# Optimization experiments

Measured on AMD Instinct MI355X. Metric: run time of the kernel, lower is better.

## Reference

```python
import jax, jax.numpy as jnp
import numpy as np

N_NODES = 40000
FEAT = 128
HID = 128
EMB = 64
N_EDGES = 640000


def setup_inputs() -> dict:
    key = jax.random.key(0)
    ks = jax.random.split(key, 8)
    x = jax.random.normal(ks[0], (N_NODES, FEAT), dtype=jnp.float32)
    edge_index = jax.random.randint(ks[1], (2, N_EDGES), 0, N_NODES, dtype=jnp.int64)
    s1 = 1.0 / np.sqrt(FEAT)
    s2 = 1.0 / np.sqrt(HID)
    W1_l = jax.random.uniform(ks[2], (HID, FEAT), jnp.float32, -s1, s1)
    b1 = jax.random.uniform(ks[3], (HID,), jnp.float32, -s1, s1)
    W1_r = jax.random.uniform(ks[4], (HID, FEAT), jnp.float32, -s1, s1)
    W2_l = jax.random.uniform(ks[5], (EMB, HID), jnp.float32, -s2, s2)
    b2 = jax.random.uniform(ks[6], (EMB,), jnp.float32, -s2, s2)
    W2_r = jax.random.uniform(ks[7], (EMB, HID), jnp.float32, -s2, s2)
    return {"x": x, "edge_index": edge_index, "W1_l": W1_l, "b1": b1,
            "W1_r": W1_r, "W2_l": W2_l, "b2": b2, "W2_r": W2_r}


def _sage_conv(x, src, dst, W_l, b_l, W_r, n_nodes):
    # mean aggregation of source-node features onto destination nodes
    msg = x[src]                                           # [E, d]
    agg = jax.ops.segment_sum(msg, dst, num_segments=n_nodes)   # [N, d]
    cnt = jax.ops.segment_sum(jnp.ones((src.shape[0],), x.dtype), dst,
                              num_segments=n_nodes)        # [N]
    agg = agg / jnp.maximum(cnt, 1.0)[:, None]
    # out = lin_l(mean_j x_j) + lin_r(x_i); bias lives in lin_l
    return agg @ W_l.T + b_l + x @ W_r.T


def reference(x, edge_index, W1_l, b1, W1_r, W2_l, b2, W2_r):
    src, dst = edge_index[0], edge_index[1]
    n = x.shape[0]
    h = _sage_conv(x, src, dst, W1_l, b1, W1_r, n)
    h = jax.nn.elu(h)
    # dropout p=0.2 is identity in eval mode
    h = _sage_conv(h, src, dst, W2_l, b2, W2_r, n)
    return jax.nn.log_softmax(h, axis=1)
```

## Files before the change

kernel.cpp:

```cpp
#include <hip/hip_runtime.h>
#include <hip/hip_fp16.h>
#include <math.h>

#define N_NODES 40000
#define FEATD 128
#define EMB 64
#define N_EDGES 640000
#define CAP 64
#define NB 79
#define BINCAP 10240

typedef unsigned short u16;
typedef unsigned char u8;
typedef unsigned int u32;
typedef __attribute__((ext_vector_type(8))) unsigned short u16x8;
typedef __attribute__((ext_vector_type(8))) _Float16 f16x8;
typedef __attribute__((ext_vector_type(4))) float f32x4;
typedef __attribute__((ext_vector_type(2))) float f32x2;
typedef __attribute__((ext_vector_type(2))) unsigned int u32x2;

__device__ __forceinline__ float h2f(u16 h) {
  __half hh;
  *(u16*)&hh = h;
  return __half2float(hh);
}
__device__ __forceinline__ u16 f2h(float f) {
  __half hh = __float2half(f);
  return *(u16*)&hh;
}

__global__ __launch_bounds__(256) void prep_fill_kernel(
    const float* __restrict__ x, const float* __restrict__ W1l,
    const float* __restrict__ W1r, const float* __restrict__ W2l,
    const float* __restrict__ W2r, const int* __restrict__ src,
    const int* __restrict__ dst, u16* __restrict__ xh, u8* __restrict__ xq,
    u16* __restrict__ wp, u32* __restrict__ binstore, int* __restrict__ binCnt) {
  __shared__ int hist[NB], starts[NB + 1], cnt2[NB], gbase[NB];
  __shared__ u32 staging[1024];
  int bid = blockIdx.x;
  int tid = threadIdx.x;
  if (bid < 625) {
    if (tid < NB) { hist[tid] = 0; cnt2[tid] = 0; }
    __syncthreads();
    int t = bid * 256 + tid;
    int4 s4 = *(const int4*)(&src[t * 4]);
    int4 d4 = *(const int4*)(&dst[t * 4]);
    int b0 = d4.x >> 9, b1 = d4.y >> 9, b2 = d4.z >> 9, b3 = d4.w >> 9;
    atomicAdd(&hist[b0], 1); atomicAdd(&hist[b1], 1);
    atomicAdd(&hist[b2], 1); atomicAdd(&hist[b3], 1);
    __syncthreads();
    if (tid == 0) {
      int run = 0;
      for (int i = 0; i < NB; i++) { starts[i] = run; run += hist[i]; }
      starts[NB] = run;
    }
    __syncthreads();
    u32 e0 = ((u32)d4.x << 16) | (u32)s4.x;
    u32 e1 = ((u32)d4.y << 16) | (u32)s4.y;
    u32 e2 = ((u32)d4.z << 16) | (u32)s4.z;
    u32 e3 = ((u32)d4.w << 16) | (u32)s4.w;
    int p0 = starts[b0] + atomicAdd(&cnt2[b0], 1); staging[p0] = e0;
    int p1 = starts[b1] + atomicAdd(&cnt2[b1], 1); staging[p1] = e1;
    int p2 = starts[b2] + atomicAdd(&cnt2[b2], 1); staging[p2] = e2;
    int p3 = starts[b3] + atomicAdd(&cnt2[b3], 1); staging[p3] = e3;
    __syncthreads();
    if (tid < NB) gbase[tid] = atomicAdd(&binCnt[tid * 16], hist[tid]);
    __syncthreads();
#pragma unroll
    for (int it = 0; it < 4; it++) {
      int i = tid + 256 * it;
      u32 e = staging[i];
      int b = (int)(e >> 25);
      int g = gbase[b] + (i - starts[b]);
      if (g < BINCAP) binstore[(size_t)b * BINCAP + g] = e;
    }
  } else if (bid < 3125) {
    int i = (bid - 625) * 256 + tid;
    float4 v0 = *(const float4*)(&x[i * 8]);
    float4 v1 = *(const float4*)(&x[i * 8 + 4]);
    u16x8 o;
    o[0] = f2h(v0.x); o[1] = f2h(v0.y); o[2] = f2h(v0.z); o[3] = f2h(v0.w);
    o[4] = f2h(v1.x); o[5] = f2h(v1.y); o[6] = f2h(v1.z); o[7] = f2h(v1.w);
    *(u16x8*)(&xh[i * 8]) = o;
    u32 w0 = __builtin_amdgcn_cvt_pk_fp8_f32(v0.x, v0.y, 0u, false);
    w0 = __builtin_amdgcn_cvt_pk_fp8_f32(v0.z, v0.w, w0, true);
    u32 w1 = __builtin_amdgcn_cvt_pk_fp8_f32(v1.x, v1.y, 0u, false);
    w1 = __builtin_amdgcn_cvt_pk_fp8_f32(v1.z, v1.w, w1, true);
    u32x2 qo; qo.x = w0; qo.y = w1;
    *(u32x2*)(&xq[i * 8]) = qo;
  } else {
    int i = (bid - 3125) * 256 + tid;
    const float* srcp;
    int off;
    if (i < 16384)      { srcp = W1l; off = i; }
    else if (i < 32768) { srcp = W1r; off = i - 16384; }
    else if (i < 40960) { srcp = W2l; off = i - 32768; }
    else                { srcp = W2r; off = i - 40960; }
    wp[i] = f2h(srcp[off]);
  }
}

__global__ __launch_bounds__(512) void scatter_kernel(
    const u32* __restrict__ binstore, const int* __restrict__ binCnt,
    int* __restrict__ deg, u16* __restrict__ bucket) {
  __shared__ int ldeg[512];
  int b = blockIdx.x, tid = threadIdx.x;
  ldeg[tid] = 0;
  __syncthreads();
  int cnt = binCnt[b * 16];
  if (cnt > BINCAP) cnt = BINCAP;
  int n0 = b << 9;
  const u32* bs = binstore + (size_t)b * BINCAP;
  int i = tid;
  for (; i + 1536 < cnt; i += 2048) {
    u32 e0 = bs[i], e1 = bs[i + 512], e2 = bs[i + 1024], e3 = bs[i + 1536];
    int l0 = (int)(e0 >> 16) - n0, l1 = (int)(e1 >> 16) - n0;
    int l2 = (int)(e2 >> 16) - n0, l3 = (int)(e3 >> 16) - n0;
    int s0 = atomicAdd(&ldeg[l0], 1);
    int s1 = atomicAdd(&ldeg[l1], 1);
    int s2 = atomicAdd(&ldeg[l2], 1);
    int s3 = atomicAdd(&ldeg[l3], 1);
    if (s0 < CAP) bucket[(size_t)(n0 + l0) * CAP + s0] = (u16)(e0 & 0xffff);
    if (s1 < CAP) bucket[(size_t)(n0 + l1) * CAP + s1] = (u16)(e1 & 0xffff);
    if (s2 < CAP) bucket[(size_t)(n0 + l2) * CAP + s2] = (u16)(e2 & 0xffff);
    if (s3 < CAP) bucket[(size_t)(n0 + l3) * CAP + s3] = (u16)(e3 & 0xffff);
  }
  for (; i < cnt; i += 512) {
    u32 e = bs[i];
    int l = (int)(e >> 16) - n0;
    int s = atomicAdd(&ldeg[l], 1);
    if (s < CAP) bucket[(size_t)(n0 + l) * CAP + s] = (u16)(e & 0xffff);
  }
  __syncthreads();
  int n = n0 + tid;
  if (n < N_NODES) deg[n] = ldeg[tid];
}

__global__ __launch_bounds__(256) void gather_mean_f8(
    const u8* __restrict__ xq, const int* __restrict__ deg,
    const u16* __restrict__ bucket, u16* __restrict__ aggh) {
  int n = blockIdx.x * 4 + (threadIdx.x >> 6);
  int lane = threadIdx.x & 63;
  int g = lane >> 4;
  int li = lane & 15;
  int dgf = deg[n];
  int dg = dgf < CAP ? dgf : CAP;
  float inv = 1.0f / fmaxf((float)dgf, 1.0f);
  const u16* bk = bucket + n * CAP;
  float acc0[8], acc1[8], acc2[8], acc3[8];
#pragma unroll
  for (int i = 0; i < 8; i++) { acc0[i] = 0.f; acc1[i] = 0.f; acc2[i] = 0.f; acc3[i] = 0.f; }
  int d = g;
  for (; d + 12 < dg; d += 16) {
    u32x2 v0 = *(const u32x2*)(&xq[(size_t)bk[d] * 128 + li * 8]);
    u32x2 v1 = *(const u32x2*)(&xq[(size_t)bk[d + 4] * 128 + li * 8]);
    u32x2 v2 = *(const u32x2*)(&xq[(size_t)bk[d + 8] * 128 + li * 8]);
    u32x2 v3 = *(const u32x2*)(&xq[(size_t)bk[d + 12] * 128 + li * 8]);
    {
      f32x2 p0 = __builtin_amdgcn_cvt_pk_f32_fp8(v0.x, false);
      f32x2 p1 = __builtin_amdgcn_cvt_pk_f32_fp8(v0.x, true);
      f32x2 p2 = __builtin_amdgcn_cvt_pk_f32_fp8(v0.y, false);
      f32x2 p3 = __builtin_amdgcn_cvt_pk_f32_fp8(v0.y, true);
      acc0[0] += p0.x; acc0[1] += p0.y; acc0[2] += p1.x; acc0[3] += p1.y;
      acc0[4] += p2.x; acc0[5] += p2.y; acc0[6] += p3.x; acc0[7] += p3.y;
    }
    {
      f32x2 p0 = __builtin_amdgcn_cvt_pk_f32_fp8(v1.x, false);
      f32x2 p1 = __builtin_amdgcn_cvt_pk_f32_fp8(v1.x, true);
      f32x2 p2 = __builtin_amdgcn_cvt_pk_f32_fp8(v1.y, false);
      f32x2 p3 = __builtin_amdgcn_cvt_pk_f32_fp8(v1.y, true);
      acc1[0] += p0.x; acc1[1] += p0.y; acc1[2] += p1.x; acc1[3] += p1.y;
      acc1[4] += p2.x; acc1[5] += p2.y; acc1[6] += p3.x; acc1[7] += p3.y;
    }
    {
      f32x2 p0 = __builtin_amdgcn_cvt_pk_f32_fp8(v2.x, false);
      f32x2 p1 = __builtin_amdgcn_cvt_pk_f32_fp8(v2.x, true);
      f32x2 p2 = __builtin_amdgcn_cvt_pk_f32_fp8(v2.y, false);
      f32x2 p3 = __builtin_amdgcn_cvt_pk_f32_fp8(v2.y, true);
      acc2[0] += p0.x; acc2[1] += p0.y; acc2[2] += p1.x; acc2[3] += p1.y;
      acc2[4] += p2.x; acc2[5] += p2.y; acc2[6] += p3.x; acc2[7] += p3.y;
    }
    {
      f32x2 p0 = __builtin_amdgcn_cvt_pk_f32_fp8(v3.x, false);
      f32x2 p1 = __builtin_amdgcn_cvt_pk_f32_fp8(v3.x, true);
      f32x2 p2 = __builtin_amdgcn_cvt_pk_f32_fp8(v3.y, false);
      f32x2 p3 = __builtin_amdgcn_cvt_pk_f32_fp8(v3.y, true);
      acc3[0] += p0.x; acc3[1] += p0.y; acc3[2] += p1.x; acc3[3] += p1.y;
      acc3[4] += p2.x; acc3[5] += p2.y; acc3[6] += p3.x; acc3[7] += p3.y;
    }
  }
  for (; d + 4 < dg; d += 8) {
    u32x2 v0 = *(const u32x2*)(&xq[(size_t)bk[d] * 128 + li * 8]);
    u32x2 v1 = *(const u32x2*)(&xq[(size_t)bk[d + 4] * 128 + li * 8]);
    {
      f32x2 p0 = __builtin_amdgcn_cvt_pk_f32_fp8(v0.x, false);
      f32x2 p1 = __builtin_amdgcn_cvt_pk_f32_fp8(v0.x, true);
      f32x2 p2 = __builtin_amdgcn_cvt_pk_f32_fp8(v0.y, false);
      f32x2 p3 = __builtin_amdgcn_cvt_pk_f32_fp8(v0.y, true);
      acc0[0] += p0.x; acc0[1] += p0.y; acc0[2] += p1.x; acc0[3] += p1.y;
      acc0[4] += p2.x; acc0[5] += p2.y; acc0[6] += p3.x; acc0[7] += p3.y;
    }
    {
      f32x2 p0 = __builtin_amdgcn_cvt_pk_f32_fp8(v1.x, false);
      f32x2 p1 = __builtin_amdgcn_cvt_pk_f32_fp8(v1.x, true);
      f32x2 p2 = __builtin_amdgcn_cvt_pk_f32_fp8(v1.y, false);
      f32x2 p3 = __builtin_amdgcn_cvt_pk_f32_fp8(v1.y, true);
      acc1[0] += p0.x; acc1[1] += p0.y; acc1[2] += p1.x; acc1[3] += p1.y;
      acc1[4] += p2.x; acc1[5] += p2.y; acc1[6] += p3.x; acc1[7] += p3.y;
    }
  }
  if (d < dg) {
    u32x2 v0 = *(const u32x2*)(&xq[(size_t)bk[d] * 128 + li * 8]);
    f32x2 p0 = __builtin_amdgcn_cvt_pk_f32_fp8(v0.x, false);
    f32x2 p1 = __builtin_amdgcn_cvt_pk_f32_fp8(v0.x, true);
    f32x2 p2 = __builtin_amdgcn_cvt_pk_f32_fp8(v0.y, false);
    f32x2 p3 = __builtin_amdgcn_cvt_pk_f32_fp8(v0.y, true);
    acc0[0] += p0.x; acc0[1] += p0.y; acc0[2] += p1.x; acc0[3] += p1.y;
    acc0[4] += p2.x; acc0[5] += p2.y; acc0[6] += p3.x; acc0[7] += p3.y;
  }
#pragma unroll
  for (int i = 0; i < 8; i++) {
    acc0[i] += acc1[i] + acc2[i] + acc3[i];
    acc0[i] += __shfl_xor(acc0[i], 16);
    acc0[i] += __shfl_xor(acc0[i], 32);
  }
  if (g == 0) {
    u16x8 o;
#pragma unroll
    for (int i = 0; i < 8; i++) o[i] = f2h(acc0[i] * inv);
    *(u16x8*)(&aggh[n * 128 + li * 8]) = o;
  }
}

__global__ __launch_bounds__(256) void gemm12_kernel(
    const u16* __restrict__ AggH, const u16* __restrict__ XH,
    const u16* __restrict__ wp, const float* __restrict__ b1v,
    const float* __restrict__ b2v, u8* __restrict__ Yq,
    u16* __restrict__ Zh) {
  const u16* w1l = wp;
  const u16* w1r = wp + 16384;
  const u16* w2l = wp + 32768;
  const u16* w2r = wp + 40960;

  __shared__ __align__(16) union {
    struct {
      u16 wl[128][72], wr[128][72];
      u16 a[64][72], x[64][72];
    } p1;
    struct {
      u16 h[64][136];
      u16 w2l[64][136], w2r[64][136];
    } p2;
  } L;

  const int tid = threadIdx.x;
  const int wv = tid >> 6;
  const int lane = tid & 63;
  const int li = lane & 15;
  const int q = lane >> 4;
  const int nbase = blockIdx.x * 64;

  f32x4 acc1[8];
#pragma unroll
  for (int jt = 0; jt < 8; jt++) acc1[jt] = (f32x4){0.f, 0.f, 0.f, 0.f};

  for (int kb = 0; kb < 2; kb++) {
#pragma unroll
    for (int it = 0; it < 4; it++) {
      int idx = tid + 256 * it;
      int j = idx >> 3, c = idx & 7;
      int go = j * 128 + kb * 64 + c * 8;
      *(u16x8*)(&L.p1.wl[j][c * 8]) = *(const u16x8*)(&w1l[go]);
      *(u16x8*)(&L.p1.wr[j][c * 8]) = *(const u16x8*)(&w1r[go]);
    }
#pragma unroll
    for (int it = 0; it < 2; it++) {
      int idx = tid + 256 * it;
      int n = idx >> 3, c = idx & 7;
      int go = (nbase + n) * 128 + kb * 64 + c * 8;
      *(u16x8*)(&L.p1.a[n][c * 8]) = *(const u16x8*)(&AggH[go]);
      *(u16x8*)(&L.p1.x[n][c * 8]) = *(const u16x8*)(&XH[go]);
    }
    __syncthreads();
#pragma unroll
    for (int kk = 0; kk < 2; kk++) {
      f16x8 aF = *(const f16x8*)(&L.p1.a[wv * 16 + li][kk * 32 + q * 8]);
      f16x8 xF = *(const f16x8*)(&L.p1.x[wv * 16 + li][kk * 32 + q * 8]);
#pragma unroll
      for (int jt = 0; jt < 8; jt++) {
        f16x8 wlF = *(const f16x8*)(&L.p1.wl[jt * 16 + li][kk * 32 + q * 8]);
        f16x8 wrF = *(const f16x8*)(&L.p1.wr[jt * 16 + li][kk * 32 + q * 8]);
        acc1[jt] = __builtin_amdgcn_mfma_f32_16x16x32_f16(aF, wlF, acc1[jt], 0, 0, 0);
        acc1[jt] = __builtin_amdgcn_mfma_f32_16x16x32_f16(xF, wrF, acc1[jt], 0, 0, 0);
      }
    }
    __syncthreads();
  }

#pragma unroll
  for (int jt = 0; jt < 8; jt++) {
    int j = jt * 16 + li;
    float bb = b1v[j];
#pragma unroll
    for (int r = 0; r < 4; r++) {
      float v = acc1[jt][r] + bb;
      v = v > 0.f ? v : expm1f(v);
      L.p2.h[wv * 16 + q * 4 + r][j] = f2h(v);
    }
  }
#pragma unroll
  for (int it = 0; it < 4; it++) {
    int idx = tid + 256 * it;
    int j = idx >> 4, c = idx & 15;
    int go = j * 128 + c * 8;
    *(u16x8*)(&L.p2.w2l[j][c * 8]) = *(const u16x8*)(&w2l[go]);
    *(u16x8*)(&L.p2.w2r[j][c * 8]) = *(const u16x8*)(&w2r[go]);
  }
  __syncthreads();

  f32x4 accY[4], accZ[4];
#pragma unroll
  for (int mt = 0; mt < 4; mt++) {
    accY[mt] = (f32x4){0.f, 0.f, 0.f, 0.f};
    accZ[mt] = (f32x4){0.f, 0.f, 0.f, 0.f};
  }
#pragma unroll
  for (int kc = 0; kc < 4; kc++) {
    f16x8 blF = *(const f16x8*)(&L.p2.w2l[wv * 16 + li][kc * 32 + q * 8]);
    f16x8 brF = *(const f16x8*)(&L.p2.w2r[wv * 16 + li][kc * 32 + q * 8]);
#pragma unroll
    for (int mt = 0; mt < 4; mt++) {
      f16x8 hF = *(const f16x8*)(&L.p2.h[mt * 16 + li][kc * 32 + q * 8]);
      accY[mt] = __builtin_amdgcn_mfma_f32_16x16x32_f16(hF, blF, accY[mt], 0, 0, 0);
      accZ[mt] = __builtin_amdgcn_mfma_f32_16x16x32_f16(hF, brF, accZ[mt], 0, 0, 0);
    }
  }

  {
    int j2 = wv * 16 + li;
    float bb = b2v[j2];
#pragma unroll
    for (int mt = 0; mt < 4; mt++) {
#pragma unroll
      for (int r = 0; r < 4; r++) {
        int node = nbase + mt * 16 + q * 4 + r;
        float yv = accY[mt][r];
        u32 w = __builtin_amdgcn_cvt_pk_fp8_f32(yv, yv, 0u, false);
        Yq[node * 64 + j2] = (u8)w;
        Zh[node * 64 + j2] = f2h(accZ[mt][r] + bb);
      }
    }
  }
}

__global__ __launch_bounds__(256) void final_kernel(
    const u8* __restrict__ Yq, const u16* __restrict__ Zh,
    const int* __restrict__ deg, const u16* __restrict__ bucket,
    float* __restrict__ out) {
  int n = blockIdx.x * 4 + (threadIdx.x >> 6);
  int lane = threadIdx.x & 63;
  int g = lane >> 3;
  int li = lane & 7;
  int dgf = deg[n];
  int dg = dgf < CAP ? dgf : CAP;
  float inv = 1.0f / fmaxf((float)dgf, 1.0f);
  const u16* bk = bucket + n * CAP;
  float acc0[8], acc1[8];
#pragma unroll
  for (int i = 0; i < 8; i++) { acc0[i] = 0.f; acc1[i] = 0.f; }
  int d = g;
  for (; d + 8 < dg; d += 16) {
    u32x2 v0 = *(const u32x2*)(&Yq[(size_t)bk[d] * 64 + li * 8]);
    u32x2 v1 = *(const u32x2*)(&Yq[(size_t)bk[d + 8] * 64 + li * 8]);
    {
      f32x2 p0 = __builtin_amdgcn_cvt_pk_f32_fp8(v0.x, false);
      f32x2 p1 = __builtin_amdgcn_cvt_pk_f32_fp8(v0.x, true);
      f32x2 p2 = __builtin_amdgcn_cvt_pk_f32_fp8(v0.y, false);
      f32x2 p3 = __builtin_amdgcn_cvt_pk_f32_fp8(v0.y, true);
      acc0[0] += p0.x; acc0[1] += p0.y; acc0[2] += p1.x; acc0[3] += p1.y;
      acc0[4] += p2.x; acc0[5] += p2.y; acc0[6] += p3.x; acc0[7] += p3.y;
    }
    {
      f32x2 p0 = __builtin_amdgcn_cvt_pk_f32_fp8(v1.x, false);
      f32x2 p1 = __builtin_amdgcn_cvt_pk_f32_fp8(v1.x, true);
      f32x2 p2 = __builtin_amdgcn_cvt_pk_f32_fp8(v1.y, false);
      f32x2 p3 = __builtin_amdgcn_cvt_pk_f32_fp8(v1.y, true);
      acc1[0] += p0.x; acc1[1] += p0.y; acc1[2] += p1.x; acc1[3] += p1.y;
      acc1[4] += p2.x; acc1[5] += p2.y; acc1[6] += p3.x; acc1[7] += p3.y;
    }
  }
  if (d < dg) {
    u32x2 v0 = *(const u32x2*)(&Yq[(size_t)bk[d] * 64 + li * 8]);
    f32x2 p0 = __builtin_amdgcn_cvt_pk_f32_fp8(v0.x, false);
    f32x2 p1 = __builtin_amdgcn_cvt_pk_f32_fp8(v0.x, true);
    f32x2 p2 = __builtin_amdgcn_cvt_pk_f32_fp8(v0.y, false);
    f32x2 p3 = __builtin_amdgcn_cvt_pk_f32_fp8(v0.y, true);
    acc0[0] += p0.x; acc0[1] += p0.y; acc0[2] += p1.x; acc0[3] += p1.y;
    acc0[4] += p2.x; acc0[5] += p2.y; acc0[6] += p3.x; acc0[7] += p3.y;
  }
#pragma unroll
  for (int i = 0; i < 8; i++) {
    acc0[i] += acc1[i];
    acc0[i] += __shfl_xor(acc0[i], 8);
    acc0[i] += __shfl_xor(acc0[i], 16);
    acc0[i] += __shfl_xor(acc0[i], 32);
  }
  u16x8 zb = *(const u16x8*)(&Zh[n * 64 + li * 8]);
  float v[8];
#pragma unroll
  for (int i = 0; i < 8; i++) v[i] = h2f(zb[i]) + acc0[i] * inv;
  float m = v[0];
#pragma unroll
  for (int i = 1; i < 8; i++) m = fmaxf(m, v[i]);
  m = fmaxf(m, __shfl_xor(m, 1));
  m = fmaxf(m, __shfl_xor(m, 2));
  m = fmaxf(m, __shfl_xor(m, 4));
  float s = 0.f;
#pragma unroll
  for (int i = 0; i < 8; i++) s += __expf(v[i] - m);
  s += __shfl_xor(s, 1); s += __shfl_xor(s, 2); s += __shfl_xor(s, 4);
  float lg = m + logf(s);
  if (lane < 8) {
    float4 o0 = {v[0] - lg, v[1] - lg, v[2] - lg, v[3] - lg};
    float4 o1 = {v[4] - lg, v[5] - lg, v[6] - lg, v[7] - lg};
    *(float4*)(&out[n * 64 + li * 8]) = o0;
    *(float4*)(&out[n * 64 + li * 8 + 4]) = o1;
  }
}

extern "C" void kernel_launch(void* const* d_in, const int* in_sizes, int n_in,
                              void* d_out, int out_size, void* d_ws, size_t ws_size,
                              hipStream_t stream) {
  const float* x   = (const float*)d_in[0];
  const int*   ei  = (const int*)d_in[1];
  const float* W1l = (const float*)d_in[2];
  const float* b1  = (const float*)d_in[3];
  const float* W1r = (const float*)d_in[4];
  const float* W2l = (const float*)d_in[5];
  const float* b2  = (const float*)d_in[6];
  const float* W2r = (const float*)d_in[7];
  float* out = (float*)d_out;

  const int* src = ei;
  const int* dst = ei + N_EDGES;

  u16* bucket = (u16*)d_ws;
  int* deg = (int*)(bucket + (size_t)N_NODES * CAP);
  u16* xh = (u16*)(deg + N_NODES);
  u16* aggh = xh + (size_t)N_NODES * FEATD;
  u8* xq = (u8*)(aggh + (size_t)N_NODES * FEATD);
  u8* yq = xq + (size_t)N_NODES * FEATD;
  u16* zh = (u16*)(yq + (size_t)N_NODES * EMB);
  u16* wp = zh + (size_t)N_NODES * EMB;
  u32* binstore = (u32*)(wp + 49152);
  int* binCnt = (int*)(binstore + (size_t)NB * BINCAP);

  hipMemsetAsync(binCnt, 0, NB * 16 * sizeof(int), stream);
  prep_fill_kernel<<<3317, 256, 0, stream>>>(x, W1l, W1r, W2l, W2r, src, dst,
                                             xh, xq, wp, binstore, binCnt);
  scatter_kernel<<<NB, 512, 0, stream>>>(binstore, binCnt, deg, bucket);
  gather_mean_f8<<<N_NODES / 4, 256, 0, stream>>>(xq, deg, bucket, aggh);
  gemm12_kernel<<<N_NODES / 64, 256, 0, stream>>>(aggh, xh, wp, b1, b2, yq, zh);
  final_kernel<<<N_NODES / 4, 256, 0, stream>>>(yq, zh, deg, bucket, out);
}
```

Baseline: 166.7 us.

## Replace global atomic bin counters with per-block edge segments and counts

Each fill block now writes its binned edges into a private fixed-size segment per bin and records per-bin counts, which removes the global atomicAdd on bin counters and the memset that preceded it. The serial prefix scan is replaced by a parallel Hillis-Steele scan in shared memory. The scatter kernel now has each thread walk one block's segment serially. Work per thread is uneven and each thread reads its segment sequentially, so loads are less coalesced. Edges beyond SEGCAP in a segment are silently dropped.

Result: no change. 163.7 us (median of 2 runs) (-1.8%).

```diff
diff --git a/kernel.cpp b/kernel.cpp
--- a/kernel.cpp
+++ b/kernel.cpp
@@ -8,7 +8,8 @@
 #define N_EDGES 640000
 #define CAP 64
 #define NB 79
-#define BINCAP 10240
+#define NFB 625
+#define SEGCAP 48
 
 typedef unsigned short u16;
 typedef unsigned char u8;
@@ -34,12 +35,12 @@
     const float* __restrict__ W1r, const float* __restrict__ W2l,
     const float* __restrict__ W2r, const int* __restrict__ src,
     const int* __restrict__ dst, u16* __restrict__ xh, u8* __restrict__ xq,
-    u16* __restrict__ wp, u32* __restrict__ binstore, int* __restrict__ binCnt) {
-  __shared__ int hist[NB], starts[NB + 1], cnt2[NB], gbase[NB];
+    u16* __restrict__ wp, u32* __restrict__ est, u16* __restrict__ cnts) {
+  __shared__ int hist[NB], starts[NB], scan[NB], cnt2[NB];
   __shared__ u32 staging[1024];
   int bid = blockIdx.x;
   int tid = threadIdx.x;
-  if (bid < 625) {
+  if (bid < NFB) {
     if (tid < NB) { hist[tid] = 0; cnt2[tid] = 0; }
     __syncthreads();
     int t = bid * 256 + tid;
@@ -49,11 +50,16 @@
     atomicAdd(&hist[b0], 1); atomicAdd(&hist[b1], 1);
     atomicAdd(&hist[b2], 1); atomicAdd(&hist[b3], 1);
     __syncthreads();
-    if (tid == 0) {
-      int run = 0;
-      for (int i = 0; i < NB; i++) { starts[i] = run; run += hist[i]; }
-      starts[NB] = run;
-    }
+    if (tid < NB) scan[tid] = hist[tid];
+    for (int off = 1; off < NB; off <<= 1) {
+      __syncthreads();
+      int v = 0;
+      if (tid < NB && tid >= off) v = scan[tid - off];
+      __syncthreads();
+      if (tid < NB) scan[tid] += v;
+    }
+    __syncthreads();
+    if (tid < NB) starts[tid] = scan[tid] - hist[tid];
     __syncthreads();
     u32 e0 = ((u32)d4.x << 16) | (u32)s4.x;
     u32 e1 = ((u32)d4.y << 16) | (u32)s4.y;
@@ -64,18 +70,17 @@
     int p2 = starts[b2] + atomicAdd(&cnt2[b2], 1); staging[p2] = e2;
     int p3 = starts[b3] + atomicAdd(&cnt2[b3], 1); staging[p3] = e3;
     __syncthreads();
-    if (tid < NB) gbase[tid] = atomicAdd(&binCnt[tid * 16], hist[tid]);
-    __syncthreads();
 #pragma unroll
     for (int it = 0; it < 4; it++) {
       int i = tid + 256 * it;
       u32 e = staging[i];
       int b = (int)(e >> 25);
-      int g = gbase[b] + (i - starts[b]);
-      if (g < BINCAP) binstore[(size_t)b * BINCAP + g] = e;
-    }
+      int r = i - starts[b];
+      if (r < SEGCAP) est[((size_t)b * NFB + bid) * SEGCAP + r] = e;
+    }
+    if (tid < NB) cnts[tid * NFB + bid] = (u16)hist[tid];
   } else if (bid < 3125) {
-    int i = (bid - 625) * 256 + tid;
+    int i = (bid - NFB) * 256 + tid;
     float4 v0 = *(const float4*)(&x[i * 8]);
     float4 v1 = *(const float4*)(&x[i * 8 + 4]);
     u16x8 o;
@@ -101,35 +106,23 @@
 }
 
 __global__ __launch_bounds__(512) void scatter_kernel(
-    const u32* __restrict__ binstore, const int* __restrict__ binCnt,
+    const u32* __restrict__ est, const u16* __restrict__ cnts,
     int* __restrict__ deg, u16* __restrict__ bucket) {
   __shared__ int ldeg[512];
   int b = blockIdx.x, tid = threadIdx.x;
   ldeg[tid] = 0;
   __syncthreads();
-  int cnt = binCnt[b * 16];
-  if (cnt > BINCAP) cnt = BINCAP;
   int n0 = b << 9;
-  const u32* bs = binstore + (size_t)b * BINCAP;
-  int i = tid;
-  for (; i + 1536 < cnt; i += 2048) {
-    u32 e0 = bs[i], e1 = bs[i + 512], e2 = bs[i + 1024], e3 = bs[i + 1536];
-    int l0 = (int)(e0 >> 16) - n0, l1 = (int)(e1 >> 16) - n0;
-    int l2 = (int)(e2 >> 16) - n0, l3 = (int)(e3 >> 16) - n0;
-    int s0 = atomicAdd(&ldeg[l0], 1);
-    int s1 = atomicAdd(&ldeg[l1], 1);
-    int s2 = atomicAdd(&ldeg[l2], 1);
-    int s3 = atomicAdd(&ldeg[l3], 1);
-    if (s0 < CAP) bucket[(size_t)(n0 + l0) * CAP + s0] = (u16)(e0 & 0xffff);
-    if (s1 < CAP) bucket[(size_t)(n0 + l1) * CAP + s1] = (u16)(e1 & 0xffff);
-    if (s2 < CAP) bucket[(size_t)(n0 + l2) * CAP + s2] = (u16)(e2 & 0xffff);
-    if (s3 < CAP) bucket[(size_t)(n0 + l3) * CAP + s3] = (u16)(e3 & 0xffff);
-  }
-  for (; i < cnt; i += 512) {
-    u32 e = bs[i];
-    int l = (int)(e >> 16) - n0;
-    int s = atomicAdd(&ldeg[l], 1);
-    if (s < CAP) bucket[(size_t)(n0 + l) * CAP + s] = (u16)(e & 0xffff);
+  for (int seg = tid; seg < NFB; seg += 512) {
+    int c = cnts[b * NFB + seg];
+    if (c > SEGCAP) c = SEGCAP;
+    const u32* p = est + ((size_t)b * NFB + seg) * SEGCAP;
+    for (int r = 0; r < c; r++) {
+      u32 e = p[r];
+      int l = (int)(e >> 16) - n0;
+      int s = atomicAdd(&ldeg[l], 1);
+      if (s < CAP) bucket[(size_t)(n0 + l) * CAP + s] = (u16)(e & 0xffff);
+    }
   }
   __syncthreads();
   int n = n0 + tid;
@@ -452,13 +445,12 @@
   u8* yq = xq + (size_t)N_NODES * FEATD;
   u16* zh = (u16*)(yq + (size_t)N_NODES * EMB);
   u16* wp = zh + (size_t)N_NODES * EMB;
-  u32* binstore = (u32*)(wp + 49152);
-  int* binCnt = (int*)(binstore + (size_t)NB * BINCAP);
-
-  hipMemsetAsync(binCnt, 0, NB * 16 * sizeof(int), stream);
+  u32* est = (u32*)(wp + 49152);
+  u16* cnts = (u16*)(est + (size_t)NB * NFB * SEGCAP);
+
   prep_fill_kernel<<<3317, 256, 0, stream>>>(x, W1l, W1r, W2l, W2r, src, dst,
-                                             xh, xq, wp, binstore, binCnt);
-  scatter_kernel<<<NB, 512, 0, stream>>>(binstore, binCnt, deg, bucket);
+                                             xh, xq, wp, est, cnts);
+  scatter_kernel<<<NB, 512, 0, stream>>>(est, cnts, deg, bucket);
   gather_mean_f8<<<N_NODES / 4, 256, 0, stream>>>(xq, deg, bucket, aggh);
   gemm12_kernel<<<N_NODES / 64, 256, 0, stream>>>(aggh, xh, wp, b1, b2, yq, zh);
   final_kernel<<<N_NODES / 4, 256, 0, stream>>>(yq, zh, deg, bucket, out);
```
